# Performance work log

Hardware: AMD Instinct MI355X
Metric: run time of the kernel (lower is better)

The kernel has to match this reference:

```python
import jax, jax.numpy as jnp
import numpy as np

T, E, DIM, HID = 8192, 8, 1024, 2048


def setup_inputs() -> dict:
    key = jax.random.key(0)
    k1, k2, k3 = jax.random.split(key, 3)
    x = jax.random.normal(k1, (T, DIM), dtype=jnp.float32)
    w1 = jax.random.normal(k2, (E, HID, DIM), dtype=jnp.float32)
    w2 = jax.random.normal(k3, (E, DIM, HID), dtype=jnp.float32)
    # Tokens are pre-grouped by expert; counts must sum exactly to T.
    num_tokens_per_expert = jnp.full((E,), T // E, dtype=jnp.int32)
    return {"x": x, "w1": w1, "w2": w2, "num_tokens_per_expert": num_tokens_per_expert}


def reference(x, w1, w2, num_tokens_per_expert):
    # Faithful to torch._grouped_mm path: bf16 casts, two ragged grouped GEMMs,
    # result cast back to x.dtype.
    gs = num_tokens_per_expert.astype(jnp.int32)
    xb = x.astype(jnp.bfloat16)                                  # [T, dim]
    w1t = jnp.swapaxes(w1.astype(jnp.bfloat16), -2, -1)          # [E, dim, hid]
    w2t = jnp.swapaxes(w2.astype(jnp.bfloat16), -2, -1)          # [E, hid, dim]
    h = jax.lax.ragged_dot(xb, w1t, gs)                          # [T, hid] bf16
    out = jax.lax.ragged_dot(h, w2t, gs)                         # [T, dim] bf16
    return out.astype(x.dtype)
```

## Files before the change

### kernel.cpp

```cpp
#include <hip/hip_runtime.h>
#include <stdint.h>

#define T_TOK 8192
#define NEXP  8
#define DIMSZ 1024
#define HIDSZ 2048

typedef __attribute__((ext_vector_type(4))) float f32x4;
typedef __attribute__((ext_vector_type(8))) short s16x8;


__device__ __forceinline__ uint16_t f2bf(float f) {
  uint32_t u = __builtin_bit_cast(uint32_t, f);
  u += 0x7fffu + ((u >> 16) & 1u);
  return (uint16_t)(u >> 16);
}

__device__ __forceinline__ uint32_t pkbf(float a, float b) {
  return (uint32_t)f2bf(a) | ((uint32_t)f2bf(b) << 16);
}

__device__ __forceinline__ void cvt_unit(const float* __restrict__ src,
                                         uint16_t* __restrict__ dst, size_t j) {
  const float4* p = (const float4*)src + 4 * j;
  float4 a = p[0], b = p[1], c = p[2], d = p[3];
  uint4 o0, o1;
  o0.x = pkbf(a.x, a.y); o0.y = pkbf(a.z, a.w);
  o0.z = pkbf(b.x, b.y); o0.w = pkbf(b.z, b.w);
  o1.x = pkbf(c.x, c.y); o1.y = pkbf(c.z, c.w);
  o1.z = pkbf(d.x, d.y); o1.w = pkbf(d.z, d.w);
  uint4* q = (uint4*)dst + 2 * j;
  q[0] = o0;
  q[1] = o1;
}

__device__ __forceinline__ void gload_lds16(const uint16_t* g, const uint16_t* lds_base) {
  __builtin_amdgcn_global_load_lds(
      (const __attribute__((address_space(1))) uint32_t*)(uintptr_t)g,
      (__attribute__((address_space(3))) uint32_t*)(uint32_t)(uintptr_t)lds_base,
      16, 0, 0);
}

__device__ __forceinline__ s16x8 ds_read128(const uint16_t* addr) {
  s16x8 r;
  asm volatile("ds_read_b128 %0, %1"
               : "=v"(r)
               : "v"((uint32_t)(uintptr_t)addr));
  return r;
}


__global__ void cvt_xw1(const float* __restrict__ x, const float* __restrict__ w1,
                        uint16_t* __restrict__ xb, uint16_t* __restrict__ w1b,
                        const int* __restrict__ counts, int* __restrict__ offs,
                        int* __restrict__ toffs) {
  if (blockIdx.x == 0 && threadIdx.x == 0) {
    int s = 0, ts = 0;
    for (int e = 0; e < NEXP; ++e) {
      offs[e] = s; toffs[e] = ts;
      s += counts[e]; ts += (counts[e] + 127) >> 7;
    }
    offs[NEXP] = s; toffs[NEXP] = ts;
  }
  const int NX = (T_TOK * DIMSZ) / 16;
  const int NW = (NEXP * HIDSZ * DIMSZ) / 16;
  const int total = NX + NW;
  const int stride = gridDim.x * blockDim.x;
  for (int i = blockIdx.x * blockDim.x + threadIdx.x; i < total; i += stride) {
    if (i < NX) cvt_unit(x, xb, i);
    else        cvt_unit(w1, w1b, i - NX);
  }
}

template <bool OUT_BF16>
__global__ __launch_bounds__(256, 2)
void gemm_grouped(const uint16_t* __restrict__ A, const uint16_t* __restrict__ B,
                  void* __restrict__ C, const int* __restrict__ offs,
                  const int* __restrict__ toffs, int N, int K, int lognt,
                  const float* __restrict__ cvt_src, uint16_t* __restrict__ cvt_dst,
                  int ncvt, int cvt_units) {
  __shared__ __align__(16) uint16_t As0[128 * 64];
  __shared__ __align__(16) uint16_t Bs0[128 * 64];
  __shared__ __align__(16) uint16_t As1[128 * 64];
  __shared__ __align__(16) uint16_t Bs1[128 * 64];

  const int nb = gridDim.x - ncvt;

  if ((int)blockIdx.x >= nb) {
    const int cb = blockIdx.x - nb;
    const int cstride = ncvt * 256;
    for (int u = cb * 256 + threadIdx.x; u < cvt_units; u += cstride)
      cvt_unit(cvt_src, cvt_dst, u);
    return;
  }

  const int orig = blockIdx.x;
  const int qc = nb >> 3, rc = nb & 7, xcd = orig & 7;
  const int bid = (xcd < rc ? xcd * (qc + 1) : rc * (qc + 1) + (xcd - rc) * qc) + (orig >> 3);

  const int mtg = bid >> lognt;
  const int nt  = bid & ((1 << lognt) - 1);
  if (mtg >= toffs[NEXP]) return;
  int e = 0;
#pragma unroll
  for (int i = 1; i < NEXP; ++i) e += (toffs[i] <= mtg) ? 1 : 0;
  const int mt      = mtg - toffs[e];
  const int m_start = offs[e];
  const int m_count = offs[e + 1] - m_start;
  const int m0      = mt * 128;
  int valid_m = m_count - m0;
  if (valid_m > 128) valid_m = 128;
  const int n0 = nt * 128;

  const int tid  = threadIdx.x;
  const int w    = tid >> 6;
  const int lane = tid & 63;
  const int wm = w & 1, wn = w >> 1;

  const uint16_t* gA = A + (size_t)m_start * K;
  const uint16_t* gB = B + (size_t)e * N * K;

  const uint16_t* ap[4];
  const uint16_t* bp[4];
#pragma unroll
  for (int c = 0; c < 4; ++c) {
    const int r  = w * 32 + c * 8 + (lane >> 3);
    const int q8 = ((lane & 7) ^ ((r >> 1) & 7)) * 8;
    const int ra = (r < valid_m) ? r : (valid_m - 1);
    ap[c] = gA + (size_t)(m0 + ra) * K + q8;
    bp[c] = gB + (size_t)(n0 + r) * K + q8;
  }

  const int fr = lane & 15;
  const int f0 = ((lane >> 4) ^ ((fr >> 1) & 7)) * 8;

  f32x4 acc[4][4];
#pragma unroll
  for (int mi = 0; mi < 4; ++mi)
#pragma unroll
    for (int ni = 0; ni < 4; ++ni) acc[mi][ni] = (f32x4){0.f, 0.f, 0.f, 0.f};

  const int NT = K >> 6;

#pragma unroll
  for (int c = 0; c < 4; ++c) {
    gload_lds16(ap[c], &As0[(w * 32 + c * 8) * 64]);
    gload_lds16(bp[c], &Bs0[(w * 32 + c * 8) * 64]);
    ap[c] += 64; bp[c] += 64;
  }
  asm volatile("s_waitcnt vmcnt(0)" ::: "memory");
  __builtin_amdgcn_s_barrier();
  __builtin_amdgcn_sched_barrier(0);

#define GSTEP(CURA, CURB, NXTA, NXTB, MORE)                                    \
  {                                                                            \
    if (MORE) {                                                                \
      _Pragma("unroll")                                                        \
      for (int c = 0; c < 4; ++c) {                                            \
        gload_lds16(ap[c], &NXTA[(w * 32 + c * 8) * 64]);                      \
        gload_lds16(bp[c], &NXTB[(w * 32 + c * 8) * 64]);                      \
        ap[c] += 64; bp[c] += 64;                                              \
      }                                                                        \
    }                                                                          \
    __builtin_amdgcn_sched_barrier(0);                                         \
    _Pragma("unroll")                                                          \
    for (int kk = 0; kk < 2; ++kk) {                                           \
      const int fk = f0 ^ (kk << 5);                                           \
      s16x8 af[4], bf[4];                                                      \
      _Pragma("unroll")                                                        \
      for (int mi = 0; mi < 4; ++mi)                                           \
        af[mi] = ds_read128(&CURA[(wm * 64 + mi * 16 + fr) * 64 + fk]);        \
      _Pragma("unroll")                                                        \
      for (int ni = 0; ni < 4; ++ni)                                           \
        bf[ni] = ds_read128(&CURB[(wn * 64 + ni * 16 + fr) * 64 + fk]);        \
      asm volatile("s_waitcnt lgkmcnt(0)" ::: "memory");                       \
      __builtin_amdgcn_sched_barrier(0);                                       \
      _Pragma("unroll")                                                        \
      for (int mi = 0; mi < 4; ++mi)                                           \
        _Pragma("unroll")                                                      \
        for (int ni = 0; ni < 4; ++ni)                                         \
          acc[mi][ni] = __builtin_amdgcn_mfma_f32_16x16x32_bf16(               \
              af[mi], bf[ni], acc[mi][ni], 0, 0, 0);                           \
    }                                                                          \
    if (MORE) {                                                                \
      asm volatile("s_waitcnt vmcnt(0)" ::: "memory");                         \
      __builtin_amdgcn_s_barrier();                                            \
      __builtin_amdgcn_sched_barrier(0);                                       \
    }                                                                          \
  }

  for (int t = 0; t < NT; t += 2) {
    GSTEP(As0, Bs0, As1, Bs1, (t + 1 < NT));
    GSTEP(As1, Bs1, As0, Bs0, (t + 2 < NT));
  }
#undef GSTEP

  const int cq = (lane >> 4) * 4;
  const int cc = lane & 15;
#pragma unroll
  for (int mi = 0; mi < 4; ++mi) {
#pragma unroll
    for (int r = 0; r < 4; ++r) {
      const int rt = wm * 64 + mi * 16 + cq + r;
      if (rt < valid_m) {
        const size_t rowoff = (size_t)(m_start + m0 + rt) * N;
#pragma unroll
        for (int ni = 0; ni < 4; ++ni) {
          const int col = n0 + wn * 64 + ni * 16 + cc;
          const float v = acc[mi][ni][r];
          if (OUT_BF16) {
            ((uint16_t*)C)[rowoff + col] = f2bf(v);
          } else {
            const uint32_t b = (uint32_t)f2bf(v) << 16;
            ((float*)C)[rowoff + col] = __builtin_bit_cast(float, b);
          }
        }
      }
    }
  }
}


extern "C" void kernel_launch(void* const* d_in, const int* in_sizes, int n_in,
                              void* d_out, int out_size, void* d_ws, size_t ws_size,
                              hipStream_t stream) {
  const float* x  = (const float*)d_in[0];
  const float* w1 = (const float*)d_in[1];
  const float* w2 = (const float*)d_in[2];
  const int* cnt  = (const int*)d_in[3];
  float* out = (float*)d_out;

  char* ws = (char*)d_ws;
  uint16_t* xb  = (uint16_t*)(ws);
  uint16_t* w1b = (uint16_t*)(ws + 16777216);
  uint16_t* w2b = (uint16_t*)(ws + 50331648);
  uint16_t* h   = (uint16_t*)(ws + 83886080);
  int* offs     = (int*)(ws + 117440512);
  int* toffs    = offs + 9;

  cvt_xw1<<<2048, 256, 0, stream>>>(x, w1, xb, w1b, cnt, offs, toffs);

  const int MAX_MT = T_TOK / 128 + NEXP - 1;
  const int NCVT   = 512;
  const int W2U    = (NEXP * DIMSZ * HIDSZ) / 16;

  gemm_grouped<true><<<MAX_MT * 16 + NCVT, 256, 0, stream>>>(
      xb, w1b, (void*)h, offs, toffs, HIDSZ, DIMSZ, 4, w2, w2b, NCVT, W2U);

  gemm_grouped<false><<<MAX_MT * 8, 256, 0, stream>>>(
      h, w2b, (void*)out, offs, toffs, DIMSZ, HIDSZ, 3, (const float*)nullptr,
      (uint16_t*)nullptr, 0, 0);
}
```

Baseline: 280.5 us.

## Use 256-row tiles with 512-thread blocks and deeper async load pipeline

Grouped GEMM tiles grow from 128x128 to 256xBN (BN=256 for the first GEMM, 128 for the second), using 8 waves per block, and the expert tile offsets now count 256-row tiles. The main loop issues the next stage's global-to-LDS loads right after a barrier and waits with a partial vmcnt instead of draining everything, so loads overlap compute more. The aim is more data reuse per block and fewer exposed load stalls. In exchange it uses more LDS and registers, launches fewer blocks (risking lower occupancy and uneven tail work), and pads ragged experts more heavily.

Result: slower. 444.5 us (+58.5%).

```diff
diff --git a/kernel.cpp b/kernel.cpp
--- a/kernel.cpp
+++ b/kernel.cpp
@@ -58,7 +58,7 @@
     int s = 0, ts = 0;
     for (int e = 0; e < NEXP; ++e) {
       offs[e] = s; toffs[e] = ts;
-      s += counts[e]; ts += (counts[e] + 127) >> 7;
+      s += counts[e]; ts += (counts[e] + 255) >> 8;
     }
     offs[NEXP] = s; toffs[NEXP] = ts;
   }
@@ -72,24 +72,27 @@
   }
 }
 
-template <bool OUT_BF16>
-__global__ __launch_bounds__(256, 2)
-void gemm_grouped(const uint16_t* __restrict__ A, const uint16_t* __restrict__ B,
-                  void* __restrict__ C, const int* __restrict__ offs,
-                  const int* __restrict__ toffs, int N, int K, int lognt,
-                  const float* __restrict__ cvt_src, uint16_t* __restrict__ cvt_dst,
-                  int ncvt, int cvt_units) {
-  __shared__ __align__(16) uint16_t As0[128 * 64];
-  __shared__ __align__(16) uint16_t Bs0[128 * 64];
-  __shared__ __align__(16) uint16_t As1[128 * 64];
-  __shared__ __align__(16) uint16_t Bs1[128 * 64];
+template <bool OUT_BF16, int BN>
+__global__ __launch_bounds__(512, 2)
+void gemm_big(const uint16_t* __restrict__ A, const uint16_t* __restrict__ B,
+              void* __restrict__ C, const int* __restrict__ offs,
+              const int* __restrict__ toffs, int N, int K,
+              const float* __restrict__ cvt_src, uint16_t* __restrict__ cvt_dst,
+              int ncvt, int cvt_units) {
+  constexpr int NBC = BN / 64;
+  constexpr int L   = 4 + NBC;
+  constexpr int NR  = (BN / 2) / 16;
+  __shared__ __align__(16) uint16_t As0[256 * 64];
+  __shared__ __align__(16) uint16_t As1[256 * 64];
+  __shared__ __align__(16) uint16_t Bs0[BN * 64];
+  __shared__ __align__(16) uint16_t Bs1[BN * 64];
 
   const int nb = gridDim.x - ncvt;
 
   if ((int)blockIdx.x >= nb) {
     const int cb = blockIdx.x - nb;
-    const int cstride = ncvt * 256;
-    for (int u = cb * 256 + threadIdx.x; u < cvt_units; u += cstride)
+    const int cstride = ncvt * 512;
+    for (int u = cb * 512 + threadIdx.x; u < cvt_units; u += cstride)
       cvt_unit(cvt_src, cvt_dst, u);
     return;
   }
@@ -98,8 +101,8 @@
   const int qc = nb >> 3, rc = nb & 7, xcd = orig & 7;
   const int bid = (xcd < rc ? xcd * (qc + 1) : rc * (qc + 1) + (xcd - rc) * qc) + (orig >> 3);
 
-  const int mtg = bid >> lognt;
-  const int nt  = bid & ((1 << lognt) - 1);
+  const int mtg = bid >> 3;
+  const int nt  = bid & 7;
   if (mtg >= toffs[NEXP]) return;
   int e = 0;
 #pragma unroll
@@ -107,93 +110,118 @@
   const int mt      = mtg - toffs[e];
   const int m_start = offs[e];
   const int m_count = offs[e + 1] - m_start;
-  const int m0      = mt * 128;
+  const int m0      = mt * 256;
   int valid_m = m_count - m0;
-  if (valid_m > 128) valid_m = 128;
-  const int n0 = nt * 128;
+  if (valid_m > 256) valid_m = 256;
+  const int n0 = nt * BN;
 
   const int tid  = threadIdx.x;
   const int w    = tid >> 6;
   const int lane = tid & 63;
-  const int wm = w & 1, wn = w >> 1;
+  const int wm = w >> 1, wn = w & 1;
 
   const uint16_t* gA = A + (size_t)m_start * K;
   const uint16_t* gB = B + (size_t)e * N * K;
 
   const uint16_t* ap[4];
-  const uint16_t* bp[4];
+  const uint16_t* bp[NBC];
 #pragma unroll
   for (int c = 0; c < 4; ++c) {
     const int r  = w * 32 + c * 8 + (lane >> 3);
     const int q8 = ((lane & 7) ^ ((r >> 1) & 7)) * 8;
     const int ra = (r < valid_m) ? r : (valid_m - 1);
     ap[c] = gA + (size_t)(m0 + ra) * K + q8;
+  }
+#pragma unroll
+  for (int c = 0; c < NBC; ++c) {
+    const int r  = w * 8 * NBC + c * 8 + (lane >> 3);
+    const int q8 = ((lane & 7) ^ ((r >> 1) & 7)) * 8;
     bp[c] = gB + (size_t)(n0 + r) * K + q8;
   }
 
   const int fr = lane & 15;
   const int f0 = ((lane >> 4) ^ ((fr >> 1) & 7)) * 8;
 
-  f32x4 acc[4][4];
+  f32x4 acc[4][NR];
 #pragma unroll
   for (int mi = 0; mi < 4; ++mi)
 #pragma unroll
-    for (int ni = 0; ni < 4; ++ni) acc[mi][ni] = (f32x4){0.f, 0.f, 0.f, 0.f};
+    for (int ni = 0; ni < NR; ++ni) acc[mi][ni] = (f32x4){0.f, 0.f, 0.f, 0.f};
 
   const int NT = K >> 6;
 
-#pragma unroll
-  for (int c = 0; c < 4; ++c) {
-    gload_lds16(ap[c], &As0[(w * 32 + c * 8) * 64]);
-    gload_lds16(bp[c], &Bs0[(w * 32 + c * 8) * 64]);
-    ap[c] += 64; bp[c] += 64;
-  }
-  asm volatile("s_waitcnt vmcnt(0)" ::: "memory");
-  __builtin_amdgcn_s_barrier();
-  __builtin_amdgcn_sched_barrier(0);
-
-#define GSTEP(CURA, CURB, NXTA, NXTB, MORE)                                    \
+#define STAGE(AD, BD)                                                          \
   {                                                                            \
-    if (MORE) {                                                                \
+    _Pragma("unroll")                                                          \
+    for (int c = 0; c < 4; ++c) {                                              \
+      gload_lds16(ap[c], &AD[(w * 32 + c * 8) * 64]);                          \
+      ap[c] += 64;                                                             \
+    }                                                                          \
+    _Pragma("unroll")                                                          \
+    for (int c = 0; c < NBC; ++c) {                                            \
+      gload_lds16(bp[c], &BD[(w * 8 * NBC + c * 8) * 64]);                     \
+      bp[c] += 64;                                                             \
+    }                                                                          \
+  }
+
+#define WAITVL()                                                               \
+  {                                                                            \
+    if constexpr (L == 8) { asm volatile("s_waitcnt vmcnt(8)" ::: "memory"); } \
+    else                  { asm volatile("s_waitcnt vmcnt(6)" ::: "memory"); } \
+  }
+
+#define COMPUTE(AR, BR)                                                        \
+  _Pragma("unroll")                                                            \
+  for (int kk = 0; kk < 2; ++kk) {                                             \
+    const int fk = f0 ^ (kk << 5);                                             \
+    s16x8 af[4], bf[NR];                                                       \
+    _Pragma("unroll")                                                          \
+    for (int mi = 0; mi < 4; ++mi)                                             \
+      af[mi] = ds_read128(&AR[(wm * 64 + mi * 16 + fr) * 64 + fk]);            \
+    _Pragma("unroll")                                                          \
+    for (int ni = 0; ni < NR; ++ni)                                            \
+      bf[ni] = ds_read128(&BR[(wn * (BN / 2) + ni * 16 + fr) * 64 + fk]);      \
+    asm volatile("s_waitcnt lgkmcnt(0)" ::: "memory");                         \
+    __builtin_amdgcn_sched_barrier(0);                                         \
+    _Pragma("unroll")                                                          \
+    for (int mi = 0; mi < 4; ++mi)                                             \
       _Pragma("unroll")                                                        \
-      for (int c = 0; c < 4; ++c) {                                            \
-        gload_lds16(ap[c], &NXTA[(w * 32 + c * 8) * 64]);                      \
-        gload_lds16(bp[c], &NXTB[(w * 32 + c * 8) * 64]);                      \
-        ap[c] += 64; bp[c] += 64;                                              \
+      for (int ni = 0; ni < NR; ++ni)                                          \
+        acc[mi][ni] = __builtin_amdgcn_mfma_f32_16x16x32_bf16(                 \
+            af[mi], bf[ni], acc[mi][ni], 0, 0, 0);                             \
+  }
+
+#define GSTEP(AR, BR, T)                                                       \
+  {                                                                            \
+    COMPUTE(AR, BR)                                                            \
+    if ((T) + 1 < NT) {                                                        \
+      __builtin_amdgcn_s_barrier();            \
+      __builtin_amdgcn_sched_barrier(0);                                       \
+      if ((T) + 2 < NT) {                                                      \
+        STAGE(AR, BR)                          \
+        WAITVL()                             \
+      } else {                                                                 \
+        asm volatile("s_waitcnt vmcnt(0)" ::: "memory");                       \
       }                                                                        \
-    }                                                                          \
-    __builtin_amdgcn_sched_barrier(0);                                         \
-    _Pragma("unroll")                                                          \
-    for (int kk = 0; kk < 2; ++kk) {                                           \
-      const int fk = f0 ^ (kk << 5);                                           \
-      s16x8 af[4], bf[4];                                                      \
-      _Pragma("unroll")                                                        \
-      for (int mi = 0; mi < 4; ++mi)                                           \
-        af[mi] = ds_read128(&CURA[(wm * 64 + mi * 16 + fr) * 64 + fk]);        \
-      _Pragma("unroll")                                                        \
-      for (int ni = 0; ni < 4; ++ni)                                           \
-        bf[ni] = ds_read128(&CURB[(wn * 64 + ni * 16 + fr) * 64 + fk]);        \
-      asm volatile("s_waitcnt lgkmcnt(0)" ::: "memory");                       \
-      __builtin_amdgcn_sched_barrier(0);                                       \
-      _Pragma("unroll")                                                        \
-      for (int mi = 0; mi < 4; ++mi)                                           \
-        _Pragma("unroll")                                                      \
-        for (int ni = 0; ni < 4; ++ni)                                         \
-          acc[mi][ni] = __builtin_amdgcn_mfma_f32_16x16x32_bf16(               \
-              af[mi], bf[ni], acc[mi][ni], 0, 0, 0);                           \
-    }                                                                          \
-    if (MORE) {                                                                \
-      asm volatile("s_waitcnt vmcnt(0)" ::: "memory");                         \
       __builtin_amdgcn_s_barrier();                                            \
       __builtin_amdgcn_sched_barrier(0);                                       \
     }                                                                          \
   }
 
+  STAGE(As0, Bs0)
+  STAGE(As1, Bs1)
+  WAITVL()
+  __builtin_amdgcn_s_barrier();
+  __builtin_amdgcn_sched_barrier(0);
+
   for (int t = 0; t < NT; t += 2) {
-    GSTEP(As0, Bs0, As1, Bs1, (t + 1 < NT));
-    GSTEP(As1, Bs1, As0, Bs0, (t + 2 < NT));
+    GSTEP(As0, Bs0, t);
+    GSTEP(As1, Bs1, t + 1);
   }
 #undef GSTEP
+#undef COMPUTE
+#undef WAITVL
+#undef STAGE
 
   const int cq = (lane >> 4) * 4;
   const int cc = lane & 15;
@@ -205,8 +233,8 @@
       if (rt < valid_m) {
         const size_t rowoff = (size_t)(m_start + m0 + rt) * N;
 #pragma unroll
-        for (int ni = 0; ni < 4; ++ni) {
-          const int col = n0 + wn * 64 + ni * 16 + cc;
+        for (int ni = 0; ni < NR; ++ni) {
+          const int col = n0 + wn * (BN / 2) + ni * 16 + cc;
           const float v = acc[mi][ni][r];
           if (OUT_BF16) {
             ((uint16_t*)C)[rowoff + col] = f2bf(v);
@@ -240,14 +268,15 @@
 
   cvt_xw1<<<2048, 256, 0, stream>>>(x, w1, xb, w1b, cnt, offs, toffs);
 
-  const int MAX_MT = T_TOK / 128 + NEXP - 1;
-  const int NCVT   = 512;
+  const int MAX_MT = T_TOK / 256 + NEXP - 1;
+  const int NB     = MAX_MT * 8;
+  const int NCVT   = 256;
   const int W2U    = (NEXP * DIMSZ * HIDSZ) / 16;
 
-  gemm_grouped<true><<<MAX_MT * 16 + NCVT, 256, 0, stream>>>(
-      xb, w1b, (void*)h, offs, toffs, HIDSZ, DIMSZ, 4, w2, w2b, NCVT, W2U);
-
-  gemm_grouped<false><<<MAX_MT * 8, 256, 0, stream>>>(
-      h, w2b, (void*)out, offs, toffs, DIMSZ, HIDSZ, 3, (const float*)nullptr,
+  gemm_big<true, 256><<<NB + NCVT, 512, 0, stream>>>(
+      xb, w1b, (void*)h, offs, toffs, HIDSZ, DIMSZ, w2, w2b, NCVT, W2U);
+
+  gemm_big<false, 128><<<NB, 512, 0, stream>>>(
+      h, w2b, (void*)out, offs, toffs, DIMSZ, HIDSZ, (const float*)nullptr,
       (uint16_t*)nullptr, 0, 0);
 }
```
